# Performance work log

Measured on AMD Instinct MI355X. Metric: run time of the kernel, lower is better.

Reference implementation:

```python
import jax, jax.numpy as jnp
import numpy as np

B, S, E = 2, 4096, 640
H, D, G = 4, 256, 1      # n_heads, head_dim, n_kv_groups
WINDOW = 512
SCALING = 256.0 ** -0.5  # query_pre_attn_scalar ** -0.5
EPS = 1e-6


def rmsnorm(x, scale):
    # Gemma variant: weight = 1 + scale, computed in fp32 over last dim
    xf = x.astype(jnp.float32)
    var = jnp.mean(xf * xf, axis=-1, keepdims=True)
    return (xf * jax.lax.rsqrt(var + EPS) * (1.0 + scale.astype(jnp.float32))).astype(x.dtype)


def apply_rope(x, cos, sin):
    # x: [B, h, S, D]; cos/sin: [S, D]
    half = x.shape[-1] // 2
    x1, x2 = x[..., :half], x[..., half:]
    rotated = jnp.concatenate([-x2, x1], axis=-1)
    return (x * cos[None, None] + rotated * sin[None, None]).astype(x.dtype)


def setup_inputs() -> dict:
    key = jax.random.key(0)
    ks = jax.random.split(key, 6)
    x = jax.random.normal(ks[0], (B, S, E), dtype=jnp.float32)
    # weights (torch Linear weight.T layout: [in, out])
    Wq = jax.random.normal(ks[1], (E, H * D), dtype=jnp.float32) * 0.02
    Wk = jax.random.normal(ks[2], (E, G * D), dtype=jnp.float32) * 0.02
    Wv = jax.random.normal(ks[3], (E, G * D), dtype=jnp.float32) * 0.02
    Wo = jax.random.normal(ks[4], (H * D, E), dtype=jnp.float32) * 0.02
    q_scale = jnp.zeros((D,), dtype=jnp.float32)
    k_scale = jnp.zeros((D,), dtype=jnp.float32)
    # RoPE tables (theta = rope_local_base = 10000 for sliding layers)
    inv_freq = 1.0 / (10000.0 ** (jnp.arange(0, D, 2, dtype=jnp.float32) / D))
    angles = jnp.arange(S, dtype=jnp.float32)[:, None] * inv_freq[None, :]
    angles = jnp.concatenate([angles, angles], axis=1)  # [S, D]
    cos, sin = jnp.cos(angles), jnp.sin(angles)
    # causal + sliding-window mask; True = masked out
    i = jnp.arange(S)[:, None]
    j = jnp.arange(S)[None, :]
    mask = (j > i) | ((i - j) >= WINDOW)
    return {"x": x, "mask": mask, "cos": cos, "sin": sin,
            "Wq": Wq, "Wk": Wk, "Wv": Wv, "Wo": Wo,
            "q_scale": q_scale, "k_scale": k_scale}


def reference(x, mask, cos, sin, Wq, Wk, Wv, Wo, q_scale, k_scale):
    b, s, _ = x.shape
    q = (x @ Wq).reshape(b, s, H, D).transpose(0, 2, 1, 3)  # [B,H,S,D]
    k = (x @ Wk).reshape(b, s, G, D).transpose(0, 2, 1, 3)  # [B,G,S,D]
    v = (x @ Wv).reshape(b, s, G, D).transpose(0, 2, 1, 3)  # [B,G,S,D]
    q = rmsnorm(q, q_scale)
    k = rmsnorm(k, k_scale)
    q = apply_rope(q, cos, sin)
    k = apply_rope(k, cos, sin)
    # GQA: K/V have G=1 heads; broadcasting replaces repeat_interleave
    scores = (q * SCALING) @ jnp.swapaxes(k, -1, -2)  # [B,H,S,S]
    scores = jnp.where(mask[None, None], -jnp.inf, scores)
    attn = jax.nn.softmax(scores, axis=-1)
    out = attn @ v                                     # [B,H,S,D]
    out = out.transpose(0, 2, 1, 3).reshape(b, s, H * D)
    return out @ Wo
```

## Files before the change

### kernel.cpp

```cpp
#include <hip/hip_runtime.h>
#include <hip/hip_bf16.h>
#include <stdint.h>

#define BB 2
#define SS 4096
#define EE 640
#define HH 4
#define DD 256
#define WIN 512

typedef __attribute__((ext_vector_type(8))) short bv8;
typedef __attribute__((ext_vector_type(4))) float fv4;
typedef __attribute__((ext_vector_type(16))) float fv16;

__device__ __forceinline__ unsigned short f2b(float f) {
  union { float f; unsigned u; } a; a.f = f;
  unsigned r = a.u + 0x7fffu + ((a.u >> 16) & 1u);
  return (unsigned short)(r >> 16);
}
__device__ __forceinline__ float b2f(unsigned short s) {
  union { unsigned u; float f; } a; a.u = ((unsigned)s) << 16;
  return a.f;
}
__device__ __forceinline__ unsigned cvtpk(float e0, float e1) {
  unsigned r;
  asm("v_cvt_pk_bf16_f32 %0, %1, %2" : "=v"(r) : "v"(e0), "v"(e1));
  return r;
}

typedef const __attribute__((address_space(1))) unsigned int* as1u;
typedef __attribute__((address_space(3))) unsigned int* as3u;
__device__ __forceinline__ void gld16(const unsigned short* g, unsigned short* l) {
  __builtin_amdgcn_global_load_lds((as1u)(const void*)g, (as3u)(void*)l, 16, 0, 0);
}

__global__ __launch_bounds__(256) void k_cast_bf16(const float* __restrict__ src,
                                                   unsigned short* __restrict__ dst, int n4) {
  int i = blockIdx.x * 256 + threadIdx.x;
  if (i >= n4) return;
  fv4 v = ((const fv4*)src)[i];
  ushort4 o; o.x = f2b(v.x); o.y = f2b(v.y); o.z = f2b(v.z); o.w = f2b(v.w);
  ((ushort4*)dst)[i] = o;
}

template <typename T>
__global__ __launch_bounds__(256) void k_transpose_bf16(const T* __restrict__ src,
    unsigned short* __restrict__ dst, int sstride, int dstride) {
  __shared__ float tile[32][33];
  int r0 = blockIdx.x * 32, c0 = blockIdx.y * 32;
  int t = threadIdx.x;
  int rr = t >> 3, cc = (t & 7) * 4;
  const T* p = src + (size_t)(r0 + rr) * sstride + c0 + cc;
  float v[4];
  if constexpr (sizeof(T) == 4) {
    fv4 x = *(const fv4*)p;
    v[0] = x.x; v[1] = x.y; v[2] = x.z; v[3] = x.w;
  } else {
    ushort4 x = *(const ushort4*)p;
    v[0] = b2f(x.x); v[1] = b2f(x.y); v[2] = b2f(x.z); v[3] = b2f(x.w);
  }
#pragma unroll
  for (int i = 0; i < 4; ++i) tile[cc + i][rr] = v[i];
  __syncthreads();
  ushort4 o;
  o.x = f2b(tile[rr][cc + 0]); o.y = f2b(tile[rr][cc + 1]);
  o.z = f2b(tile[rr][cc + 2]); o.w = f2b(tile[rr][cc + 3]);
  *(ushort4*)(dst + (size_t)(c0 + rr) * dstride + r0 + cc) = o;
}

template <bool OUT_BF16, int BN>
__global__ __launch_bounds__(256) void k_gemm(const unsigned short* __restrict__ A,
    const unsigned short* __restrict__ Bt, void* __restrict__ Cp,
    int M, int N, int K, int nt_n) {
  __shared__ unsigned short la[128 * 32];
  __shared__ unsigned short lb[BN * 32];
  const int bid = blockIdx.x;
  const int gidx = (bid & 7) * (gridDim.x >> 3) + (bid >> 3);
  const int m0 = (gidx / nt_n) * 128, n0 = (gidx % nt_n) * BN;
  const int tid = threadIdx.x, lane = tid & 63, wave = tid >> 6;
  const int g = lane >> 4, lr = lane & 15;
  constexpr int MI = (BN == 128) ? 4 : 2;
  const int wm = (BN == 128) ? (wave >> 1) * 64 : wave * 32;
  const int wn = (BN == 128) ? (wave & 1) * 64 : 0;
  fv4 acc[MI][4] = {};
  const int srow = wave * 32 + (lane >> 2);
  const int sch = (lane & 3) * 8;
  const unsigned short* ga0 = A + (size_t)(m0 + srow) * K + sch;
  unsigned short* lad = la + wave * 1024;
  const int srowb = (BN == 128) ? srow : (wave * 16 + (lane >> 2));
  const unsigned short* gb0 = Bt + (size_t)(n0 + srowb) * K + sch;
  unsigned short* lbd = lb + ((BN == 128) ? wave * 1024 : wave * 512);
  for (int k0 = 0; k0 < K; k0 += 32) {
    __syncthreads();
    gld16(ga0 + k0, lad);
    gld16(ga0 + (size_t)16 * K + k0, lad + 512);
    gld16(gb0 + k0, lbd);
    if constexpr (BN == 128) gld16(gb0 + (size_t)16 * K + k0, lbd + 512);
    __syncthreads();
    bv8 af[MI], bf[4];
#pragma unroll
    for (int mi = 0; mi < MI; ++mi) af[mi] = *(const bv8*)(la + (wm + mi * 16 + lr) * 32 + g * 8);
#pragma unroll
    for (int ni = 0; ni < 4; ++ni) bf[ni] = *(const bv8*)(lb + (wn + ni * 16 + lr) * 32 + g * 8);
    __builtin_amdgcn_s_setprio(1);
#pragma unroll
    for (int mi = 0; mi < MI; ++mi)
#pragma unroll
      for (int ni = 0; ni < 4; ++ni)
        acc[mi][ni] = __builtin_amdgcn_mfma_f32_16x16x32_bf16(af[mi], bf[ni], acc[mi][ni], 0, 0, 0);
    __builtin_amdgcn_s_setprio(0);
  }
#pragma unroll
  for (int mi = 0; mi < MI; ++mi) {
#pragma unroll
    for (int r = 0; r < 4; ++r) {
      size_t row = (size_t)(m0 + wm + mi * 16 + g * 4 + r);
#pragma unroll
      for (int ni = 0; ni < 4; ++ni) {
        int col = n0 + wn + ni * 16 + lr;
        float val = acc[mi][ni][r];
        if constexpr (OUT_BF16)
          ((unsigned short*)Cp)[row * N + col] = f2b(val);
        else
          ((float*)Cp)[row * N + col] = val;
      }
    }
  }
}

__global__ __launch_bounds__(320) void k_normrope(const unsigned short* __restrict__ qkv,
    const float* __restrict__ cosp, const float* __restrict__ sinp,
    const float* __restrict__ qsc, const float* __restrict__ ksc,
    unsigned short* __restrict__ qo, unsigned short* __restrict__ ko) {
  int m = blockIdx.x;
  int b = m >> 12, s = m & 4095;
  int wave = threadIdx.x >> 6, lane = threadIdx.x & 63;
  bool isq = wave < 4;
  const unsigned short* src = qkv + (size_t)m * 1536 + (isq ? wave * 256 : 1024);
  const float* scp = isq ? qsc : ksc;
  int d0 = lane * 4;
  ushort4 raw = *(const ushort4*)(src + d0);
  float x0 = b2f(raw.x), x1 = b2f(raw.y), x2 = b2f(raw.z), x3 = b2f(raw.w);
  float ss = x0 * x0 + x1 * x1 + x2 * x2 + x3 * x3;
#pragma unroll
  for (int off = 1; off < 64; off <<= 1) ss += __shfl_xor(ss, off, 64);
  float rs = rsqrtf(ss * (1.0f / 256.0f) + 1e-6f);
  fv4 sc = *(const fv4*)(scp + d0);
  float n0 = x0 * rs * (1.0f + sc.x);
  float n1 = x1 * rs * (1.0f + sc.y);
  float n2 = x2 * rs * (1.0f + sc.z);
  float n3 = x3 * rs * (1.0f + sc.w);
  float p0 = __shfl_xor(n0, 32, 64);
  float p1 = __shfl_xor(n1, 32, 64);
  float p2 = __shfl_xor(n2, 32, 64);
  float p3 = __shfl_xor(n3, 32, 64);
  float sgn = (lane < 32) ? -1.0f : 1.0f;
  fv4 c4 = *(const fv4*)(cosp + (size_t)s * 256 + d0);
  fv4 s4 = *(const fv4*)(sinp + (size_t)s * 256 + d0);
  float mult = isq ? (0.0625f * 1.44269504f) : 1.0f;
  float o0 = (n0 * c4.x + sgn * p0 * s4.x) * mult;
  float o1 = (n1 * c4.y + sgn * p1 * s4.y) * mult;
  float o2 = (n2 * c4.z + sgn * p2 * s4.z) * mult;
  float o3 = (n3 * c4.w + sgn * p3 * s4.w) * mult;
  ushort4 o; o.x = f2b(o0); o.y = f2b(o1); o.z = f2b(o2); o.w = f2b(o3);
  unsigned short* dst = isq
      ? qo + ((size_t)(b * HH + wave) * SS + s) * 256 + d0
      : ko + ((size_t)b * SS + s) * 256 + d0;
  *(ushort4*)dst = o;
}

__global__ __launch_bounds__(512, 2) void k_attn(const unsigned short* __restrict__ q,
    const unsigned short* __restrict__ kg, const unsigned short* __restrict__ vtg,
    unsigned short* __restrict__ att) {
  __shared__ __align__(16) char ldsbuf[133120];
  __shared__ float lsb[4][32];
  unsigned short* kt = (unsigned short*)ldsbuf;
  unsigned short* vl = (unsigned short*)ldsbuf + 32768;
  const int bid = blockIdx.x;
  const int gidx = (bid & 7) * 32 + (bid >> 3);
  const int b = gidx >> 7;
  const int i0 = (gidx & 127) * 32;
  const int tid = threadIdx.x, wave = tid >> 6, lane = tid & 63;
  const int h = wave >> 1, ks = wave & 1;
  const int hi = lane >> 5, l31 = lane & 31;
  bv8 qf[16];
  {
    const unsigned short* qp = q + ((size_t)(b * HH + h) * SS + i0 + l31) * 256;
#pragma unroll
    for (int m = 0; m < 16; ++m) qf[m] = *(const bv8*)(qp + m * 16 + hi * 8);
  }
  fv16 po[8] = {};
  float lsp = 0.f;
  const int t0 = (i0 >= WIN) ? ((i0 - WIN + 1) >> 6) : 0;
  const int t1 = i0 >> 6;
  const unsigned short* kb = kg + (size_t)b * SS * 256;
  const unsigned short* vb = vtg + (size_t)b * 256 * SS;
  auto stageK = [&](int t, int pp) {
    const unsigned short* kbase = kb + (size_t)t * 64 * 256;
    unsigned short* dst = kt + pp * 16384;
#pragma unroll
    for (int c = 0; c < 4; ++c) {
      int slot = c * 512 + tid;
      int row = slot >> 5, s = slot & 31;
      gld16(kbase + (size_t)row * 256 + ((s ^ (row & 7)) * 8),
            dst + (c * 512 + wave * 64) * 8);
    }
  };
  auto stageV = [&](int t, int pp) {
    const unsigned short* vbase = vb + (size_t)t * 64;
    unsigned short* dst = vl + pp * 16384;
#pragma unroll
    for (int c = 0; c < 4; ++c) {
      int slot = c * 512 + tid;
      int d_ = slot >> 3, s = slot & 7;
      gld16(vbase + (size_t)d_ * SS + ((s ^ (d_ & 7)) * 8),
            dst + (c * 512 + wave * 64) * 8);
    }
  };
  stageK(t0, 0); stageV(t0, 0);
  int p = 0;
  const int krow = ks * 32 + l31;
  const int krx = krow & 7;
  const int vrx = l31 & 7;
  const float FSUB = 16.5f * 1.44269504f;
  for (int t = t0; t <= t1; ++t) {
    __syncthreads();
    if (t < t1) { stageK(t + 1, p ^ 1); stageV(t + 1, p ^ 1); }
    fv16 sa0 = {}, sa1 = {};
    const unsigned short* ktp = kt + p * 16384 + krow * 256;
    __builtin_amdgcn_s_setprio(1);
#pragma unroll
    for (int m = 0; m < 8; ++m) {
      bv8 kfa = *(const bv8*)(ktp + (((m * 2 + hi) ^ krx) * 8));
      bv8 kfb = *(const bv8*)(ktp + ((((m + 8) * 2 + hi) ^ krx) * 8));
      sa0 = __builtin_amdgcn_mfma_f32_32x32x16_bf16(kfa, qf[m], sa0, 0, 0, 0);
      sa1 = __builtin_amdgcn_mfma_f32_32x32x16_bf16(kfb, qf[m + 8], sa1, 0, 0, 0);
    }
    __builtin_amdgcn_s_setprio(0);
    fv16 sa = sa0 + sa1;
    const int jb = t * 64;
    const int kb0 = jb + ks * 32;
    const bool nm = (kb0 + 31 > i0) || (i0 + 31 - kb0 >= WIN);
    if (nm) {
      const int qa = i0 + l31;
#pragma unroll
      for (int r = 0; r < 16; ++r) {
        int j = kb0 + (r & 3) + 8 * (r >> 2) + 4 * hi;
        if (j > qa || qa - j >= WIN) sa[r] = -1e30f;
      }
    }
    unsigned a[8];
#pragma unroll
    for (int i = 0; i < 8; ++i) {
      float e0 = exp2f(sa[2 * i] - FSUB);
      float e1 = exp2f(sa[2 * i + 1] - FSUB);
      lsp += e0 + e1;
      a[i] = cvtpk(e0, e1);
    }
    const unsigned short* vlp = vl + p * 16384;
    __builtin_amdgcn_s_setprio(1);
#pragma unroll
    for (int m2 = 0; m2 < 2; ++m2) {
      auto r02 = __builtin_amdgcn_permlane32_swap(a[m2 * 4 + 0], a[m2 * 4 + 2], false, false);
      auto r13 = __builtin_amdgcn_permlane32_swap(a[m2 * 4 + 1], a[m2 * 4 + 3], false, false);
      union { unsigned u[4]; bv8 v; } pf;
      pf.u[0] = r02[0]; pf.u[1] = r13[0]; pf.u[2] = r02[1]; pf.u[3] = r13[1];
      const int slot = (ks * 4 + m2 * 2 + hi) ^ vrx;
#pragma unroll
      for (int ds_ = 0; ds_ < 8; ++ds_) {
        bv8 vf = *(const bv8*)(vlp + (ds_ * 32 + l31) * 64 + slot * 8);
        po[ds_] = __builtin_amdgcn_mfma_f32_32x32x16_bf16(vf, pf.v, po[ds_], 0, 0, 0);
      }
    }
    __builtin_amdgcn_s_setprio(0);
    p ^= 1;
  }
  float lsfull = lsp + __shfl_xor(lsp, 32, 64);
  __syncthreads();
  float* cb = (float*)ldsbuf;
  if (ks == 1) {
#pragma unroll
    for (int ds_ = 0; ds_ < 8; ++ds_)
#pragma unroll
      for (int j = 0; j < 4; ++j) {
        int d0 = ds_ * 32 + 8 * j + 4 * hi;
        fv4 v4; v4[0] = po[ds_][4 * j]; v4[1] = po[ds_][4 * j + 1];
        v4[2] = po[ds_][4 * j + 2]; v4[3] = po[ds_][4 * j + 3];
        *(fv4*)(cb + (h * 32 + l31) * 260 + d0) = v4;
      }
    if (lane < 32) lsb[h][lane] = lsfull;
  }
  __syncthreads();
  if (ks == 0) {
    float total = lsfull + lsb[h][l31];
    float inv = 1.0f / total;
    unsigned short* op = att + ((size_t)b * SS + i0 + l31) * 1024 + h * 256;
#pragma unroll
    for (int ds_ = 0; ds_ < 8; ++ds_)
#pragma unroll
      for (int j = 0; j < 4; ++j) {
        int d0 = ds_ * 32 + 8 * j + 4 * hi;
        fv4 v4 = *(const fv4*)(cb + (h * 32 + l31) * 260 + d0);
        ushort4 o;
        o.x = f2b((po[ds_][4 * j] + v4[0]) * inv);
        o.y = f2b((po[ds_][4 * j + 1] + v4[1]) * inv);
        o.z = f2b((po[ds_][4 * j + 2] + v4[2]) * inv);
        o.w = f2b((po[ds_][4 * j + 3] + v4[3]) * inv);
        *(ushort4*)(op + d0) = o;
      }
  }
}

extern "C" void kernel_launch(void* const* d_in, const int* in_sizes, int n_in,
                              void* d_out, int out_size, void* d_ws, size_t ws_size,
                              hipStream_t stream) {
  const float* x    = (const float*)d_in[0];
  const float* cosp = (const float*)d_in[2];
  const float* sinp = (const float*)d_in[3];
  const float* Wq   = (const float*)d_in[4];
  const float* Wk   = (const float*)d_in[5];
  const float* Wv   = (const float*)d_in[6];
  const float* Wo   = (const float*)d_in[7];
  const float* qsc  = (const float*)d_in[8];
  const float* ksc  = (const float*)d_in[9];
  float* out = (float*)d_out;
  char* ws = (char*)d_ws;

  unsigned short* xb   = (unsigned short*)(ws);
  unsigned short* wqkv = (unsigned short*)(ws + 10485760);
  unsigned short* wo   = (unsigned short*)(ws + 12451840);
  unsigned short* qkv  = (unsigned short*)(ws + 13762560);
  unsigned short* qb   = (unsigned short*)(ws + 38928384);
  unsigned short* kbuf = (unsigned short*)(ws + 55705600);
  unsigned short* vt   = (unsigned short*)(ws + 59899904);
  unsigned short* attb = (unsigned short*)(ws + 64094208);

  k_cast_bf16<<<5120, 256, 0, stream>>>(x, xb, 1310720);
  k_transpose_bf16<float><<<dim3(20, 32), 256, 0, stream>>>(Wq, wqkv, 1024, 640);
  k_transpose_bf16<float><<<dim3(20, 8), 256, 0, stream>>>(Wk, wqkv + 1024 * 640, 256, 640);
  k_transpose_bf16<float><<<dim3(20, 8), 256, 0, stream>>>(Wv, wqkv + 1280 * 640, 256, 640);
  k_transpose_bf16<float><<<dim3(32, 20), 256, 0, stream>>>(Wo, wo, 640, 1024);
  k_gemm<true, 128><<<768, 256, 0, stream>>>(xb, wqkv, qkv, 8192, 1536, 640, 12);
  k_normrope<<<8192, 320, 0, stream>>>(qkv, cosp, sinp, qsc, ksc, qb, kbuf);
  k_transpose_bf16<unsigned short><<<dim3(128, 8), 256, 0, stream>>>(qkv + 1280, vt, 1536, 4096);
  k_transpose_bf16<unsigned short><<<dim3(128, 8), 256, 0, stream>>>(
      qkv + (size_t)4096 * 1536 + 1280, vt + (size_t)256 * 4096, 1536, 4096);
  k_attn<<<256, 512, 0, stream>>>(qb, kbuf, vt, attb);
  k_gemm<false, 64><<<640, 256, 0, stream>>>(attb, wo, out, 8192, 640, 1024, 10);
}
```

Baseline: 132.8 us.

## Split attention blocks by head pair and drop K/V double buffering

Result: faster. 129.9 us (-2.2%).

```diff
diff --git a/kernel.cpp b/kernel.cpp
--- a/kernel.cpp
+++ b/kernel.cpp
@@ -22,10 +22,8 @@
   union { unsigned u; float f; } a; a.u = ((unsigned)s) << 16;
   return a.f;
 }
-__device__ __forceinline__ unsigned cvtpk(float e0, float e1) {
-  unsigned r;
-  asm("v_cvt_pk_bf16_f32 %0, %1, %2" : "=v"(r) : "v"(e0), "v"(e1));
-  return r;
+__device__ __forceinline__ unsigned pk2(float lo, float hi_) {
+  return (unsigned)f2b(lo) | ((unsigned)f2b(hi_) << 16);
 }
 
 typedef const __attribute__((address_space(1))) unsigned int* as1u;
@@ -169,19 +167,21 @@
   *(ushort4*)dst = o;
 }
 
-__global__ __launch_bounds__(512, 2) void k_attn(const unsigned short* __restrict__ q,
+__global__ __launch_bounds__(256, 2) void k_attn(const unsigned short* __restrict__ q,
     const unsigned short* __restrict__ kg, const unsigned short* __restrict__ vtg,
     unsigned short* __restrict__ att) {
-  __shared__ __align__(16) char ldsbuf[133120];
-  __shared__ float lsb[4][32];
-  unsigned short* kt = (unsigned short*)ldsbuf;
-  unsigned short* vl = (unsigned short*)ldsbuf + 32768;
+  __shared__ __align__(16) unsigned short kt[64 * 256];
+  __shared__ __align__(16) unsigned short vl[256 * 64];
+  __shared__ float lsb[2][32];
   const int bid = blockIdx.x;
-  const int gidx = (bid & 7) * 32 + (bid >> 3);
-  const int b = gidx >> 7;
-  const int i0 = (gidx & 127) * 32;
+  const int gidx = (bid & 7) * 64 + (bid >> 3);
+  const int b = gidx >> 8;
+  const int slab = (gidx & 255) >> 1;
+  const int hp = gidx & 1;
+  const int i0 = slab * 32;
   const int tid = threadIdx.x, wave = tid >> 6, lane = tid & 63;
-  const int h = wave >> 1, ks = wave & 1;
+  const int hl = wave >> 1, ks = wave & 1;
+  const int h = hp * 2 + hl;
   const int hi = lane >> 5, l31 = lane & 31;
   bv8 qf[16];
   {
@@ -195,51 +195,41 @@
   const int t1 = i0 >> 6;
   const unsigned short* kb = kg + (size_t)b * SS * 256;
   const unsigned short* vb = vtg + (size_t)b * 256 * SS;
-  auto stageK = [&](int t, int pp) {
-    const unsigned short* kbase = kb + (size_t)t * 64 * 256;
-    unsigned short* dst = kt + pp * 16384;
-#pragma unroll
-    for (int c = 0; c < 4; ++c) {
-      int slot = c * 512 + tid;
-      int row = slot >> 5, s = slot & 31;
-      gld16(kbase + (size_t)row * 256 + ((s ^ (row & 7)) * 8),
-            dst + (c * 512 + wave * 64) * 8);
-    }
-  };
-  auto stageV = [&](int t, int pp) {
-    const unsigned short* vbase = vb + (size_t)t * 64;
-    unsigned short* dst = vl + pp * 16384;
-#pragma unroll
-    for (int c = 0; c < 4; ++c) {
-      int slot = c * 512 + tid;
-      int d_ = slot >> 3, s = slot & 7;
-      gld16(vbase + (size_t)d_ * SS + ((s ^ (d_ & 7)) * 8),
-            dst + (c * 512 + wave * 64) * 8);
-    }
-  };
-  stageK(t0, 0); stageV(t0, 0);
-  int p = 0;
   const int krow = ks * 32 + l31;
   const int krx = krow & 7;
   const int vrx = l31 & 7;
   const float FSUB = 16.5f * 1.44269504f;
   for (int t = t0; t <= t1; ++t) {
+    if (t > t0) __syncthreads();
+    {
+      const unsigned short* kbase = kb + (size_t)t * 64 * 256;
+#pragma unroll
+      for (int c = 0; c < 8; ++c) {
+        int sid = c * 256 + tid;
+        int row = sid >> 5, s = sid & 31;
+        gld16(kbase + (size_t)row * 256 + ((s ^ (row & 7)) * 8),
+              kt + (c * 256 + wave * 64) * 8);
+      }
+      const unsigned short* vbase = vb + (size_t)t * 64;
+#pragma unroll
+      for (int c = 0; c < 8; ++c) {
+        int sid = c * 256 + tid;
+        int d_ = sid >> 3, s = sid & 7;
+        gld16(vbase + (size_t)d_ * SS + ((s ^ (d_ & 7)) * 8),
+              vl + (c * 256 + wave * 64) * 8);
+      }
+    }
     __syncthreads();
-    if (t < t1) { stageK(t + 1, p ^ 1); stageV(t + 1, p ^ 1); }
-    fv16 sa0 = {}, sa1 = {};
-    const unsigned short* ktp = kt + p * 16384 + krow * 256;
+    fv16 sa = {};
+    const unsigned short* ktp = kt + krow * 256;
     __builtin_amdgcn_s_setprio(1);
 #pragma unroll
-    for (int m = 0; m < 8; ++m) {
-      bv8 kfa = *(const bv8*)(ktp + (((m * 2 + hi) ^ krx) * 8));
-      bv8 kfb = *(const bv8*)(ktp + ((((m + 8) * 2 + hi) ^ krx) * 8));
-      sa0 = __builtin_amdgcn_mfma_f32_32x32x16_bf16(kfa, qf[m], sa0, 0, 0, 0);
-      sa1 = __builtin_amdgcn_mfma_f32_32x32x16_bf16(kfb, qf[m + 8], sa1, 0, 0, 0);
+    for (int m = 0; m < 16; ++m) {
+      bv8 kf = *(const bv8*)(ktp + (((m * 2 + hi) ^ krx) * 8));
+      sa = __builtin_amdgcn_mfma_f32_32x32x16_bf16(kf, qf[m], sa, 0, 0, 0);
     }
     __builtin_amdgcn_s_setprio(0);
-    fv16 sa = sa0 + sa1;
-    const int jb = t * 64;
-    const int kb0 = jb + ks * 32;
+    const int kb0 = t * 64 + ks * 32;
     const bool nm = (kb0 + 31 > i0) || (i0 + 31 - kb0 >= WIN);
     if (nm) {
       const int qa = i0 + l31;
@@ -255,9 +245,8 @@
       float e0 = exp2f(sa[2 * i] - FSUB);
       float e1 = exp2f(sa[2 * i + 1] - FSUB);
       lsp += e0 + e1;
-      a[i] = cvtpk(e0, e1);
-    }
-    const unsigned short* vlp = vl + p * 16384;
+      a[i] = pk2(e0, e1);
+    }
     __builtin_amdgcn_s_setprio(1);
 #pragma unroll
     for (int m2 = 0; m2 < 2; ++m2) {
@@ -268,31 +257,29 @@
       const int slot = (ks * 4 + m2 * 2 + hi) ^ vrx;
 #pragma unroll
       for (int ds_ = 0; ds_ < 8; ++ds_) {
-        bv8 vf = *(const bv8*)(vlp + (ds_ * 32 + l31) * 64 + slot * 8);
+        bv8 vf = *(const bv8*)(vl + (ds_ * 32 + l31) * 64 + slot * 8);
         po[ds_] = __builtin_amdgcn_mfma_f32_32x32x16_bf16(vf, pf.v, po[ds_], 0, 0, 0);
       }
     }
     __builtin_amdgcn_s_setprio(0);
-    p ^= 1;
   }
   float lsfull = lsp + __shfl_xor(lsp, 32, 64);
   __syncthreads();
-  float* cb = (float*)ldsbuf;
+  unsigned* cb = (unsigned*)kt;
   if (ks == 1) {
 #pragma unroll
     for (int ds_ = 0; ds_ < 8; ++ds_)
 #pragma unroll
       for (int j = 0; j < 4; ++j) {
         int d0 = ds_ * 32 + 8 * j + 4 * hi;
-        fv4 v4; v4[0] = po[ds_][4 * j]; v4[1] = po[ds_][4 * j + 1];
-        v4[2] = po[ds_][4 * j + 2]; v4[3] = po[ds_][4 * j + 3];
-        *(fv4*)(cb + (h * 32 + l31) * 260 + d0) = v4;
-      }
-    if (lane < 32) lsb[h][lane] = lsfull;
+        cb[(hl * 32 + l31) * 133 + (d0 >> 1)] = pk2(po[ds_][4 * j], po[ds_][4 * j + 1]);
+        cb[(hl * 32 + l31) * 133 + (d0 >> 1) + 1] = pk2(po[ds_][4 * j + 2], po[ds_][4 * j + 3]);
+      }
+    if (lane < 32) lsb[hl][lane] = lsfull;
   }
   __syncthreads();
   if (ks == 0) {
-    float total = lsfull + lsb[h][l31];
+    float total = lsfull + lsb[hl][l31];
     float inv = 1.0f / total;
     unsigned short* op = att + ((size_t)b * SS + i0 + l31) * 1024 + h * 256;
 #pragma unroll
@@ -300,12 +287,13 @@
 #pragma unroll
       for (int j = 0; j < 4; ++j) {
         int d0 = ds_ * 32 + 8 * j + 4 * hi;
-        fv4 v4 = *(const fv4*)(cb + (h * 32 + l31) * 260 + d0);
+        unsigned u0 = cb[(hl * 32 + l31) * 133 + (d0 >> 1)];
+        unsigned u1 = cb[(hl * 32 + l31) * 133 + (d0 >> 1) + 1];
         ushort4 o;
-        o.x = f2b((po[ds_][4 * j] + v4[0]) * inv);
-        o.y = f2b((po[ds_][4 * j + 1] + v4[1]) * inv);
-        o.z = f2b((po[ds_][4 * j + 2] + v4[2]) * inv);
-        o.w = f2b((po[ds_][4 * j + 3] + v4[3]) * inv);
+        o.x = f2b((po[ds_][4 * j] + b2f((unsigned short)(u0 & 0xffff))) * inv);
+        o.y = f2b((po[ds_][4 * j + 1] + b2f((unsigned short)(u0 >> 16))) * inv);
+        o.z = f2b((po[ds_][4 * j + 2] + b2f((unsigned short)(u1 & 0xffff))) * inv);
+        o.w = f2b((po[ds_][4 * j + 3] + b2f((unsigned short)(u1 >> 16))) * inv);
         *(ushort4*)(op + d0) = o;
       }
   }
@@ -345,6 +333,6 @@
   k_transpose_bf16<unsigned short><<<dim3(128, 8), 256, 0, stream>>>(qkv + 1280, vt, 1536, 4096);
   k_transpose_bf16<unsigned short><<<dim3(128, 8), 256, 0, stream>>>(
       qkv + (size_t)4096 * 1536 + 1280, vt + (size_t)256 * 4096, 1536, 4096);
-  k_attn<<<256, 512, 0, stream>>>(qb, kbuf, vt, attb);
+  k_attn<<<512, 256, 0, stream>>>(qb, kbuf, vt, attb);
   k_gemm<false, 64><<<640, 256, 0, stream>>>(attb, wo, out, 8192, 640, 1024, 10);
 }
```

## Restructure attention loop barriers with partial vmcnt waits and single accumulator chain

Applied to the files above, without the earlier changes.

Result: faster. 124.5 us (-6.3%).

```diff
diff --git a/kernel.cpp b/kernel.cpp
--- a/kernel.cpp
+++ b/kernel.cpp
@@ -22,10 +22,8 @@
   union { unsigned u; float f; } a; a.u = ((unsigned)s) << 16;
   return a.f;
 }
-__device__ __forceinline__ unsigned cvtpk(float e0, float e1) {
-  unsigned r;
-  asm("v_cvt_pk_bf16_f32 %0, %1, %2" : "=v"(r) : "v"(e0), "v"(e1));
-  return r;
+__device__ __forceinline__ unsigned pk2(float lo, float hi_) {
+  return (unsigned)f2b(lo) | ((unsigned)f2b(hi_) << 16);
 }
 
 typedef const __attribute__((address_space(1))) unsigned int* as1u;
@@ -218,28 +216,32 @@
     }
   };
   stageK(t0, 0); stageV(t0, 0);
+  __syncthreads();
   int p = 0;
   const int krow = ks * 32 + l31;
   const int krx = krow & 7;
   const int vrx = l31 & 7;
   const float FSUB = 16.5f * 1.44269504f;
   for (int t = t0; t <= t1; ++t) {
-    __syncthreads();
-    if (t < t1) { stageK(t + 1, p ^ 1); stageV(t + 1, p ^ 1); }
-    fv16 sa0 = {}, sa1 = {};
+    if (t > t0) __builtin_amdgcn_s_barrier();
+    if (t < t1) {
+      stageK(t + 1, p ^ 1); stageV(t + 1, p ^ 1);
+      asm volatile("s_waitcnt vmcnt(8)" ::: "memory");
+    } else {
+      asm volatile("s_waitcnt vmcnt(0)" ::: "memory");
+    }
+    __builtin_amdgcn_sched_barrier(0);
+    __builtin_amdgcn_s_barrier();
+    fv16 sa = {};
     const unsigned short* ktp = kt + p * 16384 + krow * 256;
     __builtin_amdgcn_s_setprio(1);
 #pragma unroll
-    for (int m = 0; m < 8; ++m) {
-      bv8 kfa = *(const bv8*)(ktp + (((m * 2 + hi) ^ krx) * 8));
-      bv8 kfb = *(const bv8*)(ktp + ((((m + 8) * 2 + hi) ^ krx) * 8));
-      sa0 = __builtin_amdgcn_mfma_f32_32x32x16_bf16(kfa, qf[m], sa0, 0, 0, 0);
-      sa1 = __builtin_amdgcn_mfma_f32_32x32x16_bf16(kfb, qf[m + 8], sa1, 0, 0, 0);
+    for (int m = 0; m < 16; ++m) {
+      bv8 kf = *(const bv8*)(ktp + (((m * 2 + hi) ^ krx) * 8));
+      sa = __builtin_amdgcn_mfma_f32_32x32x16_bf16(kf, qf[m], sa, 0, 0, 0);
     }
     __builtin_amdgcn_s_setprio(0);
-    fv16 sa = sa0 + sa1;
-    const int jb = t * 64;
-    const int kb0 = jb + ks * 32;
+    const int kb0 = t * 64 + ks * 32;
     const bool nm = (kb0 + 31 > i0) || (i0 + 31 - kb0 >= WIN);
     if (nm) {
       const int qa = i0 + l31;
@@ -255,7 +257,7 @@
       float e0 = exp2f(sa[2 * i] - FSUB);
       float e1 = exp2f(sa[2 * i + 1] - FSUB);
       lsp += e0 + e1;
-      a[i] = cvtpk(e0, e1);
+      a[i] = pk2(e0, e1);
     }
     const unsigned short* vlp = vl + p * 16384;
     __builtin_amdgcn_s_setprio(1);
```
